# Performance work log

Hardware: AMD Instinct MI355X
Metric: run time of the kernel (lower is better)

## Reference

```python
import jax, jax.numpy as jnp
import numpy as np

IMG_H = 512; IMG_W = 512
STRIDE = 16
C = 128
SCALES = (32.0, 64.0, 128.0)
RATIOS = (0.5, 1.0, 2.0)
A = len(SCALES) * len(RATIOS)
FH = IMG_H // STRIDE; FW = IMG_W // STRIDE
K_PROP = 2000
CROP = 14
HIDDEN = 1024


def _conv(x, w, b, stride, padding):
    y = jax.lax.conv_general_dilated(x, w, (stride, stride), padding,
                                     dimension_numbers=('NCHW', 'OIHW', 'NCHW'))
    return y + b[None, :, None, None]


def _anchors():
    s = jnp.array(SCALES, jnp.float32); r = jnp.array(RATIOS, jnp.float32)
    ws = (s[:, None] / jnp.sqrt(r)[None, :]).reshape(-1)  # [A]
    hs = (s[:, None] * jnp.sqrt(r)[None, :]).reshape(-1)
    cx = (jnp.arange(FW, dtype=jnp.float32) + 0.5) * STRIDE
    cy = (jnp.arange(FH, dtype=jnp.float32) + 0.5) * STRIDE
    CX = jnp.broadcast_to(cx[None, :, None], (FH, FW, A))
    CY = jnp.broadcast_to(cy[:, None, None], (FH, FW, A))
    W2 = ws[None, None, :] * 0.5; H2 = hs[None, None, :] * 0.5
    a = jnp.stack([CX - W2, CY - H2, CX + W2, CY + H2], axis=-1)  # x1,y1,x2,y2
    return a.reshape(-1, 4)


def _decode(deltas, anchors):
    w = anchors[:, 2] - anchors[:, 0] + 1.0
    h = anchors[:, 3] - anchors[:, 1] + 1.0
    cx = anchors[:, 0] + 0.5 * w; cy = anchors[:, 1] + 0.5 * h
    dx, dy, dw, dh = deltas[:, 0], deltas[:, 1], deltas[:, 2], deltas[:, 3]
    pcx = dx * w + cx; pcy = dy * h + cy
    pw = jnp.exp(dw) * w; ph = jnp.exp(dh) * h
    return jnp.stack([pcx - 0.5 * pw, pcy - 0.5 * ph, pcx + 0.5 * pw, pcy + 0.5 * ph], axis=1)


def _clip(b):
    return jnp.stack([jnp.clip(b[:, 0], 0.0, IMG_W - 1.0), jnp.clip(b[:, 1], 0.0, IMG_H - 1.0),
                      jnp.clip(b[:, 2], 0.0, IMG_W - 1.0), jnp.clip(b[:, 3], 0.0, IMG_H - 1.0)], axis=1)


def _nms(boxes, scores, thr, K):
    # greedy NMS; returns K kept original indices (score-sorted, padded with 0) + validity mask
    boxes = jax.lax.stop_gradient(boxes)
    scores = jax.lax.stop_gradient(scores)
    N = boxes.shape[0]
    order = jnp.argsort(-scores)
    b = boxes[order]
    x1, y1, x2, y2 = b[:, 0], b[:, 1], b[:, 2], b[:, 3]
    areas = (x2 - x1 + 1.0) * (y2 - y1 + 1.0)
    idx = jnp.arange(N)

    def body(i, supp):
        xx1 = jnp.maximum(x1[i], x1); yy1 = jnp.maximum(y1[i], y1)
        xx2 = jnp.minimum(x2[i], x2); yy2 = jnp.minimum(y2[i], y2)
        inter = jnp.maximum(xx2 - xx1 + 1.0, 0.0) * jnp.maximum(yy2 - yy1 + 1.0, 0.0)
        iou = inter / (areas[i] + areas - inter)
        return supp | (~supp[i] & (iou > thr) & (idx > i))

    supp = jax.lax.fori_loop(0, N, body, jnp.zeros((N,), bool))
    keep = ~supp
    rank = jnp.cumsum(keep) - 1
    pos = jnp.where(keep & (rank < K), rank, K)  # K is out-of-bounds -> dropped
    out = jnp.zeros((K,), jnp.int32).at[pos].set(order.astype(jnp.int32), mode='drop')
    valid = jnp.arange(K) < jnp.minimum(jnp.sum(keep), K)
    return out, valid


def _crop_resize(feat, boxes, size):
    # feat [C,H,W]; boxes [R,4] normalized (y1,x1,y2,x2); TF crop_and_resize bilinear semantics
    Cc, H, W = feat.shape
    y1, x1, y2, x2 = boxes[:, 0], boxes[:, 1], boxes[:, 2], boxes[:, 3]
    t = jnp.arange(size, dtype=feat.dtype) / (size - 1)
    ys = (y1[:, None] + t[None, :] * (y2 - y1)[:, None]) * (H - 1)  # [R,size]
    xs = (x1[:, None] + t[None, :] * (x2 - x1)[:, None]) * (W - 1)
    y0 = jnp.clip(jnp.floor(ys).astype(jnp.int32), 0, H - 1); y1i = jnp.clip(y0 + 1, 0, H - 1)
    x0 = jnp.clip(jnp.floor(xs).astype(jnp.int32), 0, W - 1); x1i = jnp.clip(x0 + 1, 0, W - 1)
    wy = (ys - y0.astype(feat.dtype))[:, :, None]  # [R,size,1]
    wx = (xs - x0.astype(feat.dtype))[:, None, :]  # [R,1,size]

    def g(yi, xi):
        return feat[:, yi[:, :, None], xi[:, None, :]]  # [C,R,size,size]

    top = g(y0, x0) * (1 - wx) + g(y0, x1i) * wx
    bot = g(y1i, x0) * (1 - wx) + g(y1i, x1i) * wx
    val = top * (1 - wy) + bot * wy
    return jnp.transpose(val, (1, 0, 2, 3))  # [R,C,size,size]


def _forward(x, bb_w, bb_b, rpn_w, rpn_b, rpn_cls_w, rpn_cls_b, rpn_reg_w, rpn_reg_b,
             fc1_w, fc1_b, fc2_w, fc2_b, cls_w, cls_b, reg_w, reg_b):
    anchors = _anchors()
    feat = jax.nn.relu(_conv(x, bb_w, bb_b, STRIDE, 'VALID'))  # [1,C,32,32]
    h = jax.nn.relu(_conv(feat, rpn_w, rpn_b, 1, 'SAME'))
    rpn_logits = _conv(h, rpn_cls_w, rpn_cls_b, 1, 'SAME').transpose(0, 2, 3, 1).reshape(1, -1, 2)
    rpn_deltas = _conv(h, rpn_reg_w, rpn_reg_b, 1, 'SAME').transpose(0, 2, 3, 1).reshape(1, -1, 4)
    scores = jax.nn.softmax(rpn_logits[0], axis=1)[:, 1]
    boxes = _clip(_decode(jax.lax.stop_gradient(rpn_deltas[0]), anchors))  # numpy round-trip -> detached
    keep, _ = _nms(boxes, scores, 0.5, K_PROP)
    props = boxes[keep]  # [K,4] x1,y1,x2,y2
    nb = props / jnp.array([IMG_W - 1.0, IMG_H - 1.0, IMG_W - 1.0, IMG_H - 1.0], props.dtype)
    nb = nb[:, jnp.array([1, 0, 3, 2])]  # y1,x1,y2,x2
    crops = _crop_resize(feat[0], nb, CROP)  # [K,C,14,14]
    crops = crops.reshape(K_PROP, C, 7, 2, 7, 2).max(axis=(3, 5))  # max_pool2d k=2
    flat = crops.reshape(K_PROP, -1)
    h1 = jax.nn.relu(flat @ fc1_w.T + fc1_b)
    h2 = jax.nn.relu(h1 @ fc2_w.T + fc2_b)
    rcnn_logits = h2 @ cls_w.T + cls_b
    rcnn_deltas = h2 @ reg_w.T + reg_b
    rscores = jax.nn.softmax(rcnn_logits, axis=1)[:, 1:2]
    dets = _clip(_decode(jax.lax.stop_gradient(rcnn_deltas), props))
    keep2, valid2 = _nms(dets, rscores[:, 0], 0.3, K_PROP)
    m = valid2[:, None].astype(dets.dtype)
    out_dets = dets[keep2] * m
    out_scores = rscores[keep2] * m
    return (rpn_logits, rpn_deltas, props, anchors, rcnn_logits, rcnn_deltas, out_dets, out_scores)


def setup_inputs():
    key = jax.random.key(0)
    ks = jax.random.split(key, 10)
    def rn(k, shape, s):
        return jax.random.normal(k, shape, jnp.float32) * s
    return {
        'x': rn(ks[0], (1, 3, IMG_H, IMG_W), 1.0),
        'bb_w': rn(ks[1], (C, 3, STRIDE, STRIDE), 0.05), 'bb_b': jnp.zeros((C,), jnp.float32),
        'rpn_w': rn(ks[2], (C, C, 3, 3), 0.05), 'rpn_b': jnp.zeros((C,), jnp.float32),
        'rpn_cls_w': rn(ks[3], (2 * A, C, 1, 1), 0.05), 'rpn_cls_b': jnp.zeros((2 * A,), jnp.float32),
        'rpn_reg_w': rn(ks[4], (4 * A, C, 1, 1), 0.01), 'rpn_reg_b': jnp.zeros((4 * A,), jnp.float32),
        'fc1_w': rn(ks[5], (HIDDEN, C * 7 * 7), 0.01), 'fc1_b': jnp.zeros((HIDDEN,), jnp.float32),
        'fc2_w': rn(ks[6], (HIDDEN, HIDDEN), 0.02), 'fc2_b': jnp.zeros((HIDDEN,), jnp.float32),
        'cls_w': rn(ks[7], (2, HIDDEN), 0.02), 'cls_b': jnp.zeros((2,), jnp.float32),
        'reg_w': rn(ks[8], (4, HIDDEN), 0.01), 'reg_b': jnp.zeros((4,), jnp.float32),
    }


def reference(x, bb_w, bb_b, rpn_w, rpn_b, rpn_cls_w, rpn_cls_b, rpn_reg_w, rpn_reg_b,
              fc1_w, fc1_b, fc2_w, fc2_b, cls_w, cls_b, reg_w, reg_b):
    return _forward(x, bb_w, bb_b, rpn_w, rpn_b, rpn_cls_w, rpn_cls_b, rpn_reg_w, rpn_reg_b,
                    fc1_w, fc1_b, fc2_w, fc2_b, cls_w, cls_b, reg_w, reg_b)
```

## Files before the change

### kernel.cpp

```cpp
#include <hip/hip_runtime.h>
#include <cstdint>
#include <cstddef>

#define FHW   32
#define CCH   128
#define NAq   9216
#define NW1   144
#define KP    2000
#define NW2   32
#define HID   1024
#define KFC1  6272

#define OFF_LOGITS 0
#define OFF_DELTAS 18432
#define OFF_PROPS  55296
#define OFF_ANCH   63296
#define OFF_RLOG   100160
#define OFF_RDEL   104160
#define OFF_DETS   112160
#define OFF_SC     120160

typedef unsigned long long ull;

__device__ __forceinline__ void anchor_f32(int n, float* a4){
    int a = n % 9, j = (n/9) % FHW, i = n / (9*FHW);
    const float scales[3] = {32.f, 64.f, 128.f};
    const float ratios[3] = {0.5f, 1.f, 2.f};
    float s = scales[a/3], r = ratios[a%3];
    float sq = sqrtf(r);
    float ws = s / sq, hs = s * sq;
    float cx = ((float)j + 0.5f) * 16.f, cy = ((float)i + 0.5f) * 16.f;
    float W2 = ws * 0.5f, H2 = hs * 0.5f;
    a4[0] = cx - W2; a4[1] = cy - H2; a4[2] = cx + W2; a4[3] = cy + H2;
}

__global__ void anchors_k(float* __restrict__ outA){
    int n = blockIdx.x*blockDim.x + threadIdx.x;
    if (n >= NAq) return;
    float a4[4]; anchor_f32(n, a4);
    ((float4*)outA)[n] = make_float4(a4[0], a4[1], a4[2], a4[3]);
}

__global__ void transb_k(const float* __restrict__ w, double* __restrict__ wT){
    int idx = blockIdx.x*blockDim.x + threadIdx.x;
    if (idx >= CCH*768) return;
    int oc = idx / 768, t = idx % 768;
    wT[t*CCH + oc] = (double)w[idx];
}
__global__ void transw_k(const float* __restrict__ w, double* __restrict__ wT){
    int idx = blockIdx.x*blockDim.x + threadIdx.x;
    if (idx >= CCH*CCH*9) return;
    int oc = idx / (CCH*9);
    int rem = idx % (CCH*9);
    int ic = rem / 9, p = rem % 9;
    wT[(p*CCH + ic)*CCH + oc] = (double)w[idx];
}

__global__ __launch_bounds__(128) void backbone_k(const float* __restrict__ x,
    const double* __restrict__ wT, const float* __restrict__ b,
    double* __restrict__ featD, float* __restrict__ featF){
    __shared__ double patch[768];
    int j = blockIdx.x, i = blockIdx.y, tid = threadIdx.x;
    for (int t = tid; t < 768; t += 128){
        int ch = t >> 8, rem = t & 255, r = rem >> 4, cl = rem & 15;
        patch[t] = (double)x[ch*512*512 + (i*16 + r)*512 + j*16 + cl];
    }
    __syncthreads();
    double acc = (double)b[tid];
    #pragma unroll 4
    for (int t = 0; t < 768; t++) acc += patch[t] * wT[t*CCH + tid];
    double v = fmax(acc, 0.0);
    featD[(i*FHW + j)*CCH + tid] = v;
    featF[(i*FHW + j)*CCH + tid] = (float)v;
}

__global__ __launch_bounds__(128) void rpnconv_k(const double* __restrict__ feat,
    const double* __restrict__ wT, const float* __restrict__ b,
    double* __restrict__ h){
    __shared__ double patch[9*CCH];
    int j = blockIdx.x, i = blockIdx.y, tid = threadIdx.x;
    for (int t = tid; t < 9*CCH; t += 128){
        int p = t >> 7, ic = t & 127;
        int y = i + p/3 - 1, xx = j + p%3 - 1;
        patch[t] = (y >= 0 && y < FHW && xx >= 0 && xx < FHW) ? feat[(y*FHW + xx)*CCH + ic] : 0.0;
    }
    __syncthreads();
    double acc = (double)b[tid];
    #pragma unroll 4
    for (int t = 0; t < 9*CCH; t++) acc += patch[t] * wT[t*CCH + tid];
    h[(i*FHW + j)*CCH + tid] = fmax(acc, 0.0);
}

__global__ __launch_bounds__(64) void rpnhead_k(const double* __restrict__ h,
    const float* __restrict__ wc, const float* __restrict__ bc,
    const float* __restrict__ wr, const float* __restrict__ br,
    float* __restrict__ outLog, float* __restrict__ outDel,
    float* __restrict__ boxes, float* __restrict__ scores){
    __shared__ double hv[CCH];
    __shared__ double ov[54];
    int pos = blockIdx.x, tid = threadIdx.x;
    hv[tid]      = h[pos*CCH + tid];
    hv[tid + 64] = h[pos*CCH + tid + 64];
    __syncthreads();
    if (tid < 54){
        const float* wrow; double bias;
        if (tid < 18){ wrow = wc + tid*CCH; bias = (double)bc[tid]; }
        else         { wrow = wr + (tid-18)*CCH; bias = (double)br[tid-18]; }
        double acc = bias;
        #pragma unroll 4
        for (int k = 0; k < CCH; k++) acc += hv[k] * (double)wrow[k];
        ov[tid] = acc;
    }
    __syncthreads();
    if (tid < 18) outLog[pos*18 + tid] = (float)ov[tid];
    if (tid < 36) outDel[pos*36 + tid] = (float)ov[18 + tid];
    if (tid < 9){
        int n = pos*9 + tid;
        float l0 = (float)ov[2*tid], l1 = (float)ov[2*tid+1];
        float m = fmaxf(l0, l1);
        float e0 = expf(l0 - m), e1 = expf(l1 - m);
        float s = e1 / (e0 + e1);
        float dx = (float)ov[18+4*tid+0], dy = (float)ov[18+4*tid+1];
        float dw = (float)ov[18+4*tid+2], dh = (float)ov[18+4*tid+3];
        float an[4]; anchor_f32(n, an);
        float aw = an[2] - an[0] + 1.f, ah = an[3] - an[1] + 1.f;
        float acx = an[0] + 0.5f*aw, acy = an[1] + 0.5f*ah;
        float pcx = dx*aw + acx, pcy = dy*ah + acy;
        float pw = expf(dw)*aw, ph = expf(dh)*ah;
        float x1 = pcx - 0.5f*pw, y1 = pcy - 0.5f*ph;
        float x2 = pcx + 0.5f*pw, y2 = pcy + 0.5f*ph;
        x1 = fminf(fmaxf(x1, 0.f), 511.f);  y1 = fminf(fmaxf(y1, 0.f), 511.f);
        x2 = fminf(fmaxf(x2, 0.f), 511.f);  y2 = fminf(fmaxf(y2, 0.f), 511.f);
        ((float4*)boxes)[n] = make_float4(x1, y1, x2, y2);
        scores[n] = s;
    }
}

__global__ __launch_bounds__(256) void rank_sortf(const float* __restrict__ sc,
                                                  int* __restrict__ order, int N){
    __shared__ float ss[2048];
    int i = blockIdx.x*blockDim.x + threadIdx.x;
    float mys = (i < N) ? sc[i] : -1e30f;
    int r = 0;
    for (int base = 0; base < N; base += 2048){
        int cnt = min(2048, N - base);
        __syncthreads();
        for (int t = threadIdx.x; t < cnt; t += blockDim.x) ss[t] = sc[base + t];
        __syncthreads();
        for (int j = 0; j < cnt; j++){
            float s = ss[j];
            int jg = base + j;
            r += (s > mys) || (s == mys && jg < i);
        }
    }
    if (i < N) order[r] = i;
}

__global__ void gather_sorted(const float4* __restrict__ boxes, const int* __restrict__ order,
                              float4* __restrict__ sb, int N){
    int r = blockIdx.x*blockDim.x + threadIdx.x;
    if (r < N) sb[r] = boxes[order[r]];
}

__global__ __launch_bounds__(64) void nms_maskb(const float4* __restrict__ sb,
                          ull* __restrict__ mask, int N, int Nw, float thr){
    int i = blockIdx.x;
    int lane = threadIdx.x;
    float4 bi = sb[i];
    float areai = (bi.z - bi.x + 1.f) * (bi.w - bi.y + 1.f);
    int w0 = i >> 6;
    for (int w = w0; w < Nw; w++){
        int j = w*64 + lane;
        bool sup = false;
        if (j < N && j > i){
            float4 bj = sb[j];
            float xx1 = fmaxf(bi.x, bj.x), yy1 = fmaxf(bi.y, bj.y);
            float xx2 = fminf(bi.z, bj.z), yy2 = fminf(bi.w, bj.w);
            float iw = fmaxf(xx2 - xx1 + 1.f, 0.f), ih = fmaxf(yy2 - yy1 + 1.f, 0.f);
            float inter = iw * ih;
            float areaj = (bj.z - bj.x + 1.f) * (bj.w - bj.y + 1.f);
            float iou = inter / (areai + areaj - inter);
            sup = iou > thr;
        }
        ull bits = __ballot(sup);
        if (lane == 0) mask[(size_t)i*Nw + w] = bits;
    }
}

__global__ __launch_bounds__(64) void nms_scan2(const ull* __restrict__ mask,
                          const int* __restrict__ order,
                          int* __restrict__ keep, int* __restrict__ cntOut,
                          int N, int Nw, int K, int earlyStop){
    __shared__ ull removed[NW1];
    __shared__ ull diag[64];
    __shared__ int keptIdx[64];
    int tid = threadIdx.x;
    for (int t = tid; t < Nw; t += 64) removed[t] = 0ull;
    for (int t = tid; t < K;  t += 64) keep[t] = 0;
    __syncthreads();
    int cnt = 0;
    bool done = false;
    for (int iw = 0; iw < Nw && !done; ++iw){
        int i0 = iw << 6;
        int lim = N - i0; if (lim > 64) lim = 64;
        if (tid < lim) diag[tid] = mask[(size_t)(i0 + tid)*Nw + iw];
        __syncthreads();
        ull pending = ~removed[iw];
        if (lim < 64) pending &= (1ull << lim) - 1ull;
        int nk = 0;
        while (pending){
            int b = __builtin_ctzll(pending);
            if (tid == 0 && cnt < K) keep[cnt] = order[i0 + b];
            keptIdx[nk] = i0 + b;
            nk++; cnt++;
            if (earlyStop && cnt >= K){ done = true; break; }
            pending &= ~(1ull << b);
            pending &= ~diag[b];
        }
        if (done) break;
        __syncthreads();
        for (int w = iw + 1 + tid; w < Nw; w += 64){
            ull accu = 0ull;
            int r = 0;
            for (; r + 4 <= nk; r += 4){
                ull m0 = mask[(size_t)keptIdx[r+0]*Nw + w];
                ull m1 = mask[(size_t)keptIdx[r+1]*Nw + w];
                ull m2 = mask[(size_t)keptIdx[r+2]*Nw + w];
                ull m3 = mask[(size_t)keptIdx[r+3]*Nw + w];
                accu |= (m0 | m1) | (m2 | m3);
            }
            for (; r < nk; r++) accu |= mask[(size_t)keptIdx[r]*Nw + w];
            removed[w] |= accu;
        }
        __syncthreads();
    }
    if (tid == 0) *cntOut = cnt;
}

__global__ void props_k(const float4* __restrict__ boxes, const int* __restrict__ keep1,
                        float* __restrict__ outP, float4* __restrict__ propsWs){
    int j = blockIdx.x*blockDim.x + threadIdx.x;
    if (j >= KP) return;
    float4 b = boxes[keep1[j]];
    ((float4*)outP)[j] = b;
    propsWs[j] = b;
}

__global__ __launch_bounds__(128) void croppool_k(const float* __restrict__ feat,
    const float* __restrict__ props, float* __restrict__ pooled){
    __shared__ int   sy0[14], sy1[14], sx0[14], sx1[14];
    __shared__ float swy[14], swx[14];
    int n = blockIdx.x, tid = threadIdx.x;
    const float* p = props + n*4;
    if (tid < 28){
        int s = tid % 14;
        bool isx = tid >= 14;
        float c1 = (isx ? p[0] : p[1]) / 511.f;
        float c2 = (isx ? p[2] : p[3]) / 511.f;
        float t = (float)s / 13.f;
        float v = (c1 + t * (c2 - c1)) * 31.f;
        int v0 = (int)floorf(v);
        v0 = v0 < 0 ? 0 : (v0 > 31 ? 31 : v0);
        int v1i = v0 + 1; if (v1i > 31) v1i = 31;
        float wv = v - (float)v0;
        if (isx){ sx0[s]=v0; sx1[s]=v1i; swx[s]=wv; }
        else    { sy0[s]=v0; sy1[s]=v1i; swy[s]=wv; }
    }
    __syncthreads();
    int c = tid;
    float* outr = pooled + (size_t)n*KFC1 + c*49;
    for (int py = 0; py < 7; py++){
        for (int px = 0; px < 7; px++){
            float mx = -3.402823466e38f;
            #pragma unroll
            for (int dy = 0; dy < 2; dy++){
                #pragma unroll
                for (int dx = 0; dx < 2; dx++){
                    int sy = 2*py + dy, sx = 2*px + dx;
                    int y0 = sy0[sy], y1 = sy1[sy], x0 = sx0[sx], x1 = sx1[sx];
                    float wy = swy[sy], wx = swx[sx];
                    float f00 = feat[(y0*FHW + x0)*CCH + c];
                    float f01 = feat[(y0*FHW + x1)*CCH + c];
                    float f10 = feat[(y1*FHW + x0)*CCH + c];
                    float f11 = feat[(y1*FHW + x1)*CCH + c];
                    float top = f00*(1.f - wx) + f01*wx;
                    float bot = f10*(1.f - wx) + f11*wx;
                    float val = top*(1.f - wy) + bot*wy;
                    mx = fmaxf(mx, val);
                }
            }
            outr[py*7 + px] = mx;
        }
    }
}

__global__ __launch_bounds__(256) void gemm_nt_f(const float* __restrict__ A,
    const float* __restrict__ B, const float* __restrict__ bias,
    float* __restrict__ C, int M, int N, int K){
    __shared__ float As[2][64][33];
    __shared__ float Bs[2][64][33];
    int tid = threadIdx.x;
    int tx = tid & 15, ty = tid >> 4;
    int m0 = blockIdx.y*64, n0 = blockIdx.x*64;
    int ra = tid >> 3;
    int ca = (tid & 7) << 2;
    int rb = ra + 32;
    double acc[4][4];
    #pragma unroll
    for (int r = 0; r < 4; r++)
        #pragma unroll
        for (int c = 0; c < 4; c++) acc[r][c] = 0.0;

    const float4 z4 = make_float4(0.f, 0.f, 0.f, 0.f);
    float4 av0, av1, bv0, bv1;
    int gm0 = m0 + ra, gm1 = m0 + rb;
    int gn0 = n0 + ra, gn1 = n0 + rb;

    auto fetch = [&](int k0){
        av0 = (gm0 < M) ? *(const float4*)(A + (size_t)gm0*K + k0 + ca) : z4;
        av1 = (gm1 < M) ? *(const float4*)(A + (size_t)gm1*K + k0 + ca) : z4;
        bv0 = (gn0 < N) ? *(const float4*)(B + (size_t)gn0*K + k0 + ca) : z4;
        bv1 = (gn1 < N) ? *(const float4*)(B + (size_t)gn1*K + k0 + ca) : z4;
    };
    auto stash = [&](int buf){
        As[buf][ra][ca+0]=av0.x; As[buf][ra][ca+1]=av0.y; As[buf][ra][ca+2]=av0.z; As[buf][ra][ca+3]=av0.w;
        As[buf][rb][ca+0]=av1.x; As[buf][rb][ca+1]=av1.y; As[buf][rb][ca+2]=av1.z; As[buf][rb][ca+3]=av1.w;
        Bs[buf][ra][ca+0]=bv0.x; Bs[buf][ra][ca+1]=bv0.y; Bs[buf][ra][ca+2]=bv0.z; Bs[buf][ra][ca+3]=bv0.w;
        Bs[buf][rb][ca+0]=bv1.x; Bs[buf][rb][ca+1]=bv1.y; Bs[buf][rb][ca+2]=bv1.z; Bs[buf][rb][ca+3]=bv1.w;
    };

    fetch(0);
    stash(0);
    __syncthreads();
    int nt = K >> 5;
    int cur = 0;
    for (int t = 0; t < nt; t++){
        bool more = (t + 1 < nt);
        if (more) fetch((t + 1) << 5);
        #pragma unroll
        for (int k = 0; k < 32; k++){
            float avr[4], bvr[4];
            #pragma unroll
            for (int r = 0; r < 4; r++) avr[r] = As[cur][ty*4 + r][k];
            #pragma unroll
            for (int c = 0; c < 4; c++) bvr[c] = Bs[cur][tx*4 + c][k];
            #pragma unroll
            for (int r = 0; r < 4; r++)
                #pragma unroll
                for (int c = 0; c < 4; c++) acc[r][c] += (double)avr[r]*(double)bvr[c];
        }
        if (more) stash(cur ^ 1);
        __syncthreads();
        cur ^= 1;
    }
    #pragma unroll
    for (int r = 0; r < 4; r++){
        int gm = m0 + ty*4 + r;
        if (gm >= M) continue;
        #pragma unroll
        for (int c = 0; c < 4; c++){
            int gn = n0 + tx*4 + c;
            double v = acc[r][c] + (double)bias[gn];
            C[(size_t)gm*N + gn] = (float)fmax(v, 0.0);
        }
    }
}

__global__ __launch_bounds__(64) void rcnnhead_k(const float* __restrict__ h2,
    const float* __restrict__ wcls, const float* __restrict__ bcls,
    const float* __restrict__ wreg, const float* __restrict__ breg,
    const float* __restrict__ props,
    float* __restrict__ outLog, float* __restrict__ outDel,
    float* __restrict__ dets, float* __restrict__ scores2){
    int n = blockIdx.x, tid = threadIdx.x;
    const float* hr = h2 + (size_t)n*HID;
    double s[6];
    #pragma unroll
    for (int o = 0; o < 6; o++){
        const float* wrow = (o < 2) ? (wcls + o*HID) : (wreg + (o-2)*HID);
        double a = 0.0;
        for (int k = tid; k < HID; k += 64) a += (double)hr[k] * (double)wrow[k];
        #pragma unroll
        for (int off = 32; off > 0; off >>= 1) a += __shfl_down(a, off, 64);
        s[o] = a;
    }
    if (tid == 0){
        float l0 = (float)(s[0] + (double)bcls[0]), l1 = (float)(s[1] + (double)bcls[1]);
        outLog[n*2 + 0] = l0; outLog[n*2 + 1] = l1;
        float dx = (float)(s[2] + (double)breg[0]), dy = (float)(s[3] + (double)breg[1]);
        float dw = (float)(s[4] + (double)breg[2]), dh = (float)(s[5] + (double)breg[3]);
        outDel[n*4+0] = dx; outDel[n*4+1] = dy; outDel[n*4+2] = dw; outDel[n*4+3] = dh;
        float mm = fmaxf(l0, l1);
        float e0 = expf(l0 - mm), e1 = expf(l1 - mm);
        float sc = e1 / (e0 + e1);
        scores2[n] = sc;
        const float* an = props + n*4;
        float aw = an[2]-an[0]+1.f, ah = an[3]-an[1]+1.f;
        float acx = an[0] + 0.5f*aw, acy = an[1] + 0.5f*ah;
        float pcx = dx*aw + acx, pcy = dy*ah + acy;
        float pw = expf(dw)*aw, ph = expf(dh)*ah;
        float x1 = pcx - 0.5f*pw, y1 = pcy - 0.5f*ph;
        float x2 = pcx + 0.5f*pw, y2 = pcy + 0.5f*ph;
        x1 = fminf(fmaxf(x1, 0.f), 511.f);  y1 = fminf(fmaxf(y1, 0.f), 511.f);
        x2 = fminf(fmaxf(x2, 0.f), 511.f);  y2 = fminf(fmaxf(y2, 0.f), 511.f);
        dets[n*4+0] = x1; dets[n*4+1] = y1; dets[n*4+2] = x2; dets[n*4+3] = y2;
    }
}

__global__ void finalize_k(const float4* __restrict__ dets, const float* __restrict__ scores2,
                           const int* __restrict__ keep2, const int* __restrict__ cnt2,
                           float* __restrict__ outD, float* __restrict__ outS){
    int j = blockIdx.x*blockDim.x + threadIdx.x;
    if (j >= KP) return;
    int c = *cnt2;
    float m = (j < c) ? 1.f : 0.f;
    int o = keep2[j];
    float4 d = dets[o];
    outD[j*4+0] = d.x*m; outD[j*4+1] = d.y*m; outD[j*4+2] = d.z*m; outD[j*4+3] = d.w*m;
    outS[j] = scores2[o]*m;
}

extern "C" void kernel_launch(void* const* d_in, const int* in_sizes, int n_in,
                              void* d_out, int out_size, void* d_ws, size_t ws_size,
                              hipStream_t stream) {
    const float* x     = (const float*)d_in[0];
    const float* bb_w  = (const float*)d_in[1];
    const float* bb_b  = (const float*)d_in[2];
    const float* rpn_w = (const float*)d_in[3];
    const float* rpn_b = (const float*)d_in[4];
    const float* rcw   = (const float*)d_in[5];
    const float* rcb   = (const float*)d_in[6];
    const float* rrw   = (const float*)d_in[7];
    const float* rrb   = (const float*)d_in[8];
    const float* fc1w  = (const float*)d_in[9];
    const float* fc1b  = (const float*)d_in[10];
    const float* fc2w  = (const float*)d_in[11];
    const float* fc2b  = (const float*)d_in[12];
    const float* clsw  = (const float*)d_in[13];
    const float* clsb  = (const float*)d_in[14];
    const float* regw  = (const float*)d_in[15];
    const float* regb  = (const float*)d_in[16];
    float* out = (float*)d_out;

    char* base = (char*)d_ws;
    size_t off = 0;
    auto carve = [&](size_t bytes) -> void* {
        void* r = base + off;
        off = (off + bytes + 255) & ~(size_t)255;
        return r;
    };
    double* featD   = (double*)carve((size_t)FHW*FHW*CCH*8);
    float*  featF   = (float*)carve((size_t)FHW*FHW*CCH*4);
    double* hD      = (double*)carve((size_t)FHW*FHW*CCH*8);
    double* wbTD    = (double*)carve((size_t)768*CCH*8);
    double* wTD     = (double*)carve((size_t)9*CCH*CCH*8);
    float*  propsF  = (float*)carve((size_t)KP*16);
    int*    cnt1    = (int*)carve(256);
    int*    cnt2    = (int*)carve(256);
    float*  scores2F= (float*)carve((size_t)KP*4);
    float*  dets2F  = (float*)carve((size_t)KP*16);
    int*    order2  = (int*)carve(KP*4);
    float4* sb2F    = (float4*)carve((size_t)KP*16);
    ull*    mask2   = (ull*)carve((size_t)KP*NW2*8);
    int*    keep2   = (int*)carve(KP*4);
    size_t mark = off;
    float*  boxesF  = (float*)carve((size_t)NAq*16);
    float*  scoresF = (float*)carve((size_t)NAq*4);
    int*    order1  = (int*)carve((size_t)NAq*4);
    float4* sb1F    = (float4*)carve((size_t)NAq*16);
    ull*    mask1   = (ull*)carve((size_t)NAq*NW1*8);
    int*    keep1   = (int*)carve(KP*4);
    off = mark;
    float*  pooledF = (float*)carve((size_t)KP*KFC1*4);
    float*  h1F     = (float*)carve((size_t)KP*HID*4);
    float*  h2F     = (float*)carve((size_t)KP*HID*4);
    (void)ws_size; (void)in_sizes; (void)n_in; (void)out_size;

    anchors_k<<<(NAq+255)/256, 256, 0, stream>>>(out + OFF_ANCH);
    transb_k<<<(768*CCH+255)/256, 256, 0, stream>>>(bb_w, wbTD);
    transw_k<<<(9*CCH*CCH+255)/256, 256, 0, stream>>>(rpn_w, wTD);
    backbone_k<<<dim3(FHW, FHW), 128, 0, stream>>>(x, wbTD, bb_b, featD, featF);
    rpnconv_k<<<dim3(FHW, FHW), 128, 0, stream>>>(featD, wTD, rpn_b, hD);
    rpnhead_k<<<FHW*FHW, 64, 0, stream>>>(hD, rcw, rcb, rrw, rrb,
                                          out + OFF_LOGITS, out + OFF_DELTAS, boxesF, scoresF);
    rank_sortf<<<(NAq+255)/256, 256, 0, stream>>>(scoresF, order1, NAq);
    gather_sorted<<<(NAq+255)/256, 256, 0, stream>>>((const float4*)boxesF, order1, sb1F, NAq);
    nms_maskb<<<NAq, 64, 0, stream>>>(sb1F, mask1, NAq, NW1, 0.5f);
    nms_scan2<<<1, 64, 0, stream>>>(mask1, order1, keep1, cnt1, NAq, NW1, KP, 1);
    props_k<<<(KP+255)/256, 256, 0, stream>>>((const float4*)boxesF, keep1,
                                              out + OFF_PROPS, (float4*)propsF);
    croppool_k<<<KP, 128, 0, stream>>>(featF, propsF, pooledF);
    gemm_nt_f<<<dim3(HID/64, (KP+63)/64), 256, 0, stream>>>(pooledF, fc1w, fc1b, h1F, KP, HID, KFC1);
    gemm_nt_f<<<dim3(HID/64, (KP+63)/64), 256, 0, stream>>>(h1F, fc2w, fc2b, h2F, KP, HID, HID);
    rcnnhead_k<<<KP, 64, 0, stream>>>(h2F, clsw, clsb, regw, regb, propsF,
                                      out + OFF_RLOG, out + OFF_RDEL, dets2F, scores2F);
    rank_sortf<<<(KP+255)/256, 256, 0, stream>>>(scores2F, order2, KP);
    gather_sorted<<<(KP+255)/256, 256, 0, stream>>>((const float4*)dets2F, order2, sb2F, KP);
    nms_maskb<<<KP, 64, 0, stream>>>(sb2F, mask2, KP, NW2, 0.3f);
    nms_scan2<<<1, 64, 0, stream>>>(mask2, order2, keep2, cnt2, KP, NW2, KP, 0);
    finalize_k<<<(KP+255)/256, 256, 0, stream>>>((const float4*)dets2F, scores2F, keep2, cnt2,
                                                 out + OFF_DETS, out + OFF_SC);
}
```

Baseline: 3.202 ms.

## Split-K the FC GEMMs into two halves with a separate reduction kernel

The two fully connected GEMMs now split the K dimension in two along blockIdx.z, doubling the number of blocks, and each half writes double-precision partial sums to a workspace buffer. A new reduce kernel adds the two partials, applies bias and ReLU, and writes float output. This aims to raise occupancy and parallelism on a GEMM grid of only about 512 tiles, and adds a launch bound hint. The cost is extra global traffic for the 2×2000×1024 double partial buffer, plus two extra kernel launches.

```diff
diff --git a/kernel.cpp b/kernel.cpp
--- a/kernel.cpp
+++ b/kernel.cpp
@@ -294,14 +294,16 @@
     }
 }
 
-__global__ __launch_bounds__(256) void gemm_nt_f(const float* __restrict__ A,
-    const float* __restrict__ B, const float* __restrict__ bias,
-    float* __restrict__ C, int M, int N, int K){
+__global__ __launch_bounds__(256, 4) void gemm_nt_sk(const float* __restrict__ A,
+    const float* __restrict__ B, double* __restrict__ Cpart, int M, int N, int K){
     __shared__ float As[2][64][33];
     __shared__ float Bs[2][64][33];
     int tid = threadIdx.x;
     int tx = tid & 15, ty = tid >> 4;
     int m0 = blockIdx.y*64, n0 = blockIdx.x*64;
+    int z = blockIdx.z;
+    int kHalf = K >> 1;
+    int kBeg = z * kHalf;
     int ra = tid >> 3;
     int ca = (tid & 7) << 2;
     int rb = ra + 32;
@@ -329,14 +331,14 @@
         Bs[buf][rb][ca+0]=bv1.x; Bs[buf][rb][ca+1]=bv1.y; Bs[buf][rb][ca+2]=bv1.z; Bs[buf][rb][ca+3]=bv1.w;
     };
 
-    fetch(0);
+    fetch(kBeg);
     stash(0);
     __syncthreads();
-    int nt = K >> 5;
+    int nt = kHalf >> 5;
     int cur = 0;
     for (int t = 0; t < nt; t++){
         bool more = (t + 1 < nt);
-        if (more) fetch((t + 1) << 5);
+        if (more) fetch(kBeg + ((t + 1) << 5));
         #pragma unroll
         for (int k = 0; k < 32; k++){
             float avr[4], bvr[4];
@@ -353,6 +355,7 @@
         __syncthreads();
         cur ^= 1;
     }
+    double* Cz = Cpart + (size_t)z * M * N;
     #pragma unroll
     for (int r = 0; r < 4; r++){
         int gm = m0 + ty*4 + r;
@@ -360,10 +363,18 @@
         #pragma unroll
         for (int c = 0; c < 4; c++){
             int gn = n0 + tx*4 + c;
-            double v = acc[r][c] + (double)bias[gn];
-            C[(size_t)gm*N + gn] = (float)fmax(v, 0.0);
-        }
-    }
+            Cz[(size_t)gm*N + gn] = acc[r][c];
+        }
+    }
+}
+
+__global__ void sk_reduce(const double* __restrict__ p, const float* __restrict__ bias,
+                          float* __restrict__ C, int M, int N){
+    int idx = blockIdx.x*blockDim.x + threadIdx.x;
+    if (idx >= M*N) return;
+    int n = idx % N;
+    double v = (p[idx] + p[(size_t)M*N + idx]) + (double)bias[n];
+    C[idx] = (float)fmax(v, 0.0);
 }
 
 __global__ __launch_bounds__(64) void rcnnhead_k(const float* __restrict__ h2,
@@ -474,6 +485,7 @@
     float*  pooledF = (float*)carve((size_t)KP*KFC1*4);
     float*  h1F     = (float*)carve((size_t)KP*HID*4);
     float*  h2F     = (float*)carve((size_t)KP*HID*4);
+    double* Cpart   = (double*)carve((size_t)2*KP*HID*8);
     (void)ws_size; (void)in_sizes; (void)n_in; (void)out_size;
 
     anchors_k<<<(NAq+255)/256, 256, 0, stream>>>(out + OFF_ANCH);
@@ -490,8 +502,10 @@
     props_k<<<(KP+255)/256, 256, 0, stream>>>((const float4*)boxesF, keep1,
                                               out + OFF_PROPS, (float4*)propsF);
     croppool_k<<<KP, 128, 0, stream>>>(featF, propsF, pooledF);
-    gemm_nt_f<<<dim3(HID/64, (KP+63)/64), 256, 0, stream>>>(pooledF, fc1w, fc1b, h1F, KP, HID, KFC1);
-    gemm_nt_f<<<dim3(HID/64, (KP+63)/64), 256, 0, stream>>>(h1F, fc2w, fc2b, h2F, KP, HID, HID);
+    gemm_nt_sk<<<dim3(HID/64, (KP+63)/64, 2), 256, 0, stream>>>(pooledF, fc1w, Cpart, KP, HID, KFC1);
+    sk_reduce<<<(KP*HID+255)/256, 256, 0, stream>>>(Cpart, fc1b, h1F, KP, HID);
+    gemm_nt_sk<<<dim3(HID/64, (KP+63)/64, 2), 256, 0, stream>>>(h1F, fc2w, Cpart, KP, HID, HID);
+    sk_reduce<<<(KP*HID+255)/256, 256, 0, stream>>>(Cpart, fc2b, h2F, KP, HID);
     rcnnhead_k<<<KP, 64, 0, stream>>>(h2F, clsw, clsb, regw, regb, propsF,
                                       out + OFF_RLOG, out + OFF_RDEL, dets2F, scores2F);
     rank_sortf<<<(KP+255)/256, 256, 0, stream>>>(scores2F, order2, KP);
```

Measured after the change: 12.63 ms. 294% more time.
